# Kernel optimization log

Hardware: AMD Instinct MI355X
Metric: run time of the kernel (lower is better)

## Reference

```python
import jax, jax.numpy as jnp
import numpy as np

GROUPS = 32
EPS = 1e-5

def setup_inputs() -> dict:
    key = jax.random.key(0)
    ks = jax.random.split(key, 10)
    B, H, W, C = 2, 64, 64, 512
    s = 1.0 / np.sqrt(C)
    return {
        "x": jax.random.normal(ks[0], (B, H, W, C), dtype=jnp.float32),
        "gamma": jnp.ones((C,), jnp.float32),
        "beta": jnp.zeros((C,), jnp.float32),
        "wq": jax.random.normal(ks[1], (C, C), jnp.float32) * s,
        "bq": jnp.zeros((C,), jnp.float32),
        "wk": jax.random.normal(ks[2], (C, C), jnp.float32) * s,
        "bk": jnp.zeros((C,), jnp.float32),
        "wv": jax.random.normal(ks[3], (C, C), jnp.float32) * s,
        "bv": jnp.zeros((C,), jnp.float32),
        "wp": jax.random.normal(ks[4], (C, C), jnp.float32) * s,
        "bp": jnp.zeros((C,), jnp.float32),
    }

def _group_norm(x, gamma, beta):
    B, H, W, C = x.shape
    xg = x.reshape(B, H, W, GROUPS, C // GROUPS)
    mean = jnp.mean(xg, axis=(1, 2, 4), keepdims=True)
    var = jnp.var(xg, axis=(1, 2, 4), keepdims=True)
    xg = (xg - mean) * jax.lax.rsqrt(var + EPS)
    return xg.reshape(B, H, W, C) * gamma + beta

def reference(x, gamma, beta, wq, bq, wk, bk, wv, bv, wp, bp):
    B, H, W, C = x.shape
    h_ = _group_norm(x, gamma, beta)
    # 1x1 convs are per-pixel linear maps
    q = jnp.einsum("bhwc,cd->bhwd", h_, wq) + bq
    k = jnp.einsum("bhwc,cd->bhwd", h_, wk) + bk
    v = jnp.einsum("bhwc,cd->bhwd", h_, wv) + bv
    q = q.reshape(B, H * W, C)
    k = k.reshape(B, H * W, C)
    v = v.reshape(B, H * W, C)
    scale = C ** (-0.5)
    attn = jax.nn.softmax(jnp.einsum("bqc,bkc->bqk", q, k) * scale, axis=-1)
    out = jnp.einsum("bqk,bkc->bqc", attn, v).reshape(B, H, W, C)
    proj = jnp.einsum("bhwc,cd->bhwd", out, wp) + bp
    return x + proj
```

## Files before the change

kernel.cpp:

```cpp
#include <hip/hip_runtime.h>
#include <hip/hip_bf16.h>
#include <cstdint>
#include <cstddef>

typedef __bf16 bf16;
typedef bf16 bf16x8 __attribute__((ext_vector_type(8)));
typedef bf16 bf16x4 __attribute__((ext_vector_type(4)));
typedef float floatx4 __attribute__((ext_vector_type(4)));
typedef int intx8 __attribute__((ext_vector_type(8)));
typedef int intx4 __attribute__((ext_vector_type(4)));

#define DEVI __device__ __forceinline__

#define C_  512
#define HW_ 4096
#define B_  2
#define M_  8192
#define TK  64


DEVI floatx4 mfma16(bf16x8 a, bf16x8 b, floatx4 c) {
  return __builtin_amdgcn_mfma_f32_16x16x32_bf16(a, b, c, 0, 0, 0);
}

DEVI floatx4 mfma_fp8(intx8 a, intx8 b, floatx4 c) {
  return __builtin_amdgcn_mfma_scale_f32_16x16x128_f8f6f4(a, b, c, 0, 0,
                                                          0, 127, 0, 127);
}

DEVI void gload16(const void* g, void* lds) {
  using gp = const __attribute__((address_space(1))) unsigned int*;
  using lp = __attribute__((address_space(3))) unsigned int*;
  __builtin_amdgcn_global_load_lds(
      reinterpret_cast<gp>(reinterpret_cast<uintptr_t>(g)),
      reinterpret_cast<lp>((unsigned int)(uintptr_t)lds), 16, 0, 0);
}

template <int N> DEVI void wait_vmcnt() {
  if constexpr (N == 0)       asm volatile("s_waitcnt vmcnt(0)" ::: "memory");
  else if constexpr (N == 6)  asm volatile("s_waitcnt vmcnt(6)" ::: "memory");
  else if constexpr (N == 8)  asm volatile("s_waitcnt vmcnt(8)" ::: "memory");
  else static_assert(N == 0, "unsupported vmcnt literal");
}

DEVI uint32_t f32_to_fp8(float x) {
  return (uint32_t)__builtin_amdgcn_cvt_pk_fp8_f32(x, x, 0, false) & 0xffu;
}
DEVI int pack4_fp8(float a, float b, float c, float d) {
  int pk = __builtin_amdgcn_cvt_pk_fp8_f32(a, b, 0, false);
  return __builtin_amdgcn_cvt_pk_fp8_f32(c, d, pk, true);
}

__global__ __launch_bounds__(256) void gn_part(const float* __restrict__ x,
                                               float* __restrict__ pp,
                                               float* __restrict__ l) {
  int blk = blockIdx.x;
  int t = threadIdx.x;
  if (t < 16) l[blk * 16 + t] = 0.f;
  int batch = blk >> 8;
  int pix0 = (blk & 255) * 16;
  int c4 = (t & 127) << 2;
  int ph = t >> 7;
  const float* px = x + (size_t)batch * HW_ * C_ + (size_t)(pix0 + ph) * C_ + c4;
  float s1 = 0.f, s2 = 0.f;
#pragma unroll
  for (int i = 0; i < 8; i++) {
    float4 v = *reinterpret_cast<const float4*>(px + (size_t)i * 2 * C_);
    s1 += v.x + v.y + v.z + v.w;
    s2 += v.x * v.x + v.y * v.y + v.z * v.z + v.w * v.w;
  }
  __shared__ float l1[256], l2[256];
  l1[t] = s1; l2[t] = s2;
  __syncthreads();
  if (t < 32) {
    float a = 0.f, b2 = 0.f;
#pragma unroll
    for (int j = 0; j < 4; j++) {
      a  += l1[t * 4 + j] + l1[t * 4 + j + 128];
      b2 += l2[t * 4 + j] + l2[t * 4 + j + 128];
    }
    pp[blk * 32 + t] = a;
    pp[512 * 32 + blk * 32 + t] = b2;
  }
}

__global__ __launch_bounds__(256) void finish_wtrans(
    const float* __restrict__ pp, float* __restrict__ stats,
    const float* __restrict__ wq, const float* __restrict__ wk,
    const float* __restrict__ wv, const float* __restrict__ wp,
    uint8_t* __restrict__ w8, bf16* __restrict__ wtp) {
  int t = threadIdx.x;
  if (blockIdx.x < 64) {
    int bg = blockIdx.x;
    int b = bg >> 5, g = bg & 31;
    float s1 = pp[(b * 256 + t) * 32 + g];
    float s2 = pp[512 * 32 + (b * 256 + t) * 32 + g];
    for (int off = 32; off; off >>= 1) {
      s1 += __shfl_down(s1, off);
      s2 += __shfl_down(s2, off);
    }
    __shared__ float r1[4], r2[4];
    int wid = t >> 6;
    if ((t & 63) == 0) { r1[wid] = s1; r2[wid] = s2; }
    __syncthreads();
    if (t == 0) {
      s1 = r1[0] + r1[1] + r1[2] + r1[3];
      s2 = r2[0] + r2[1] + r2[2] + r2[3];
      float inv = 1.0f / (HW_ * 16);
      float mean = s1 * inv;
      float var  = s2 * inv - mean * mean;
      stats[bg]      = mean;
      stats[64 + bg] = rsqrtf(var + 1e-5f);
    }
    return;
  }
  int id = blockIdx.x - 64;
  int z = id >> 8;
  int k0 = ((id >> 4) & 15) * 32, n0 = (id & 15) * 32;
  const float* w = (z == 0) ? wq : (z == 1) ? wk : (z == 2) ? wv : wp;
  __shared__ float tt[32][33];
  int r = t >> 5, cc = t & 31;
  for (int i = 0; i < 4; i++) {
    int rr = r + i * 8;
    tt[rr][cc] = w[(size_t)(k0 + rr) * C_ + n0 + cc];
  }
  __syncthreads();
  if (z < 3) {
    uint8_t* dst = w8 + (size_t)z * C_ * C_;
    for (int i = 0; i < 4; i++) {
      int rr = r + i * 8;
      dst[(size_t)(n0 + rr) * C_ + k0 + cc] = (uint8_t)f32_to_fp8(tt[cc][rr]);
    }
  } else {
    for (int i = 0; i < 4; i++) {
      int rr = r + i * 8;
      wtp[(size_t)(n0 + rr) * C_ + k0 + cc] = (bf16)tt[cc][rr];
    }
  }
}

__global__ __launch_bounds__(256) void gn_apply(const float* __restrict__ x,
                                                const float* __restrict__ gamma,
                                                const float* __restrict__ beta,
                                                const float* __restrict__ stats,
                                                uint8_t* __restrict__ h8) {
  int idx = blockIdx.x * 256 + threadIdx.x;
  int m  = idx >> 7;
  int c4 = (idx & 127) << 2;
  int b = m >> 12;
  int g = c4 >> 4;
  float mean = stats[(b << 5) + g];
  float rs   = stats[64 + (b << 5) + g];
  const float4 xv = *reinterpret_cast<const float4*>(x + (size_t)m * C_ + c4);
  const float4 gv = *reinterpret_cast<const float4*>(gamma + c4);
  const float4 bv = *reinterpret_cast<const float4*>(beta + c4);
  int pk = pack4_fp8((xv.x - mean) * rs * gv.x + bv.x,
                     (xv.y - mean) * rs * gv.y + bv.y,
                     (xv.z - mean) * rs * gv.z + bv.z,
                     (xv.w - mean) * rs * gv.w + bv.w);
  *reinterpret_cast<int*>(h8 + (size_t)m * C_ + c4) = pk;
}

template <int BM, int BN, int MT, int NT>
DEVI void gemm_main(const bf16* __restrict__ A, int lda,
                    const bf16* __restrict__ Bt, int ldb,
                    int K, floatx4 (&acc)[MT][NT]) {
  constexpr int WCOLS = BN / (NT * 16);
  constexpr int NLD = BM / 32 + BN / 32;
  static_assert(NLD == 6 || NLD == 8, "vmcnt literal supports 6/8");
  __shared__ __align__(16) bf16 As[2][BM * TK];
  __shared__ __align__(16) bf16 Bs[2][BN * TK];
  int tid = threadIdx.x;
  int w = tid >> 6, lane = tid & 63;
  int wrow = w / WCOLS, wcol = w % WCOLS;
  int col = lane & 15, quad = lane >> 4;
#pragma unroll
  for (int mt = 0; mt < MT; mt++)
#pragma unroll
    for (int nt = 0; nt < NT; nt++)
      acc[mt][nt] = floatx4{0.f, 0.f, 0.f, 0.f};

  auto stage = [&](int k0, bf16* as, bf16* bs) {
#pragma unroll
    for (int i = 0; i < BM / 32; i++) {
      int id = tid + i * 256;
      int r = id >> 3, wd = id & 7;
      gload16(A + (size_t)r * lda + k0 + ((wd ^ (r & 7)) << 3), as + id * 8);
    }
#pragma unroll
    for (int i = 0; i < BN / 32; i++) {
      int id = tid + i * 256;
      int r = id >> 3, wd = id & 7;
      gload16(Bt + (size_t)r * ldb + k0 + ((wd ^ (r & 7)) << 3), bs + id * 8);
    }
  };
  auto compute = [&](const bf16* sa, const bf16* sb) {
#pragma unroll
    for (int kk = 0; kk < 2; kk++) {
      bf16x8 af[MT], bfr[NT];
#pragma unroll
      for (int mt = 0; mt < MT; mt++) {
        int rA = wrow * MT * 16 + mt * 16 + col;
        af[mt] = *reinterpret_cast<const bf16x8*>(
            sa + rA * TK + (((kk * 4 + quad) ^ (rA & 7)) << 3));
      }
#pragma unroll
      for (int nt = 0; nt < NT; nt++) {
        int rB = wcol * NT * 16 + nt * 16 + col;
        bfr[nt] = *reinterpret_cast<const bf16x8*>(
            sb + rB * TK + (((kk * 4 + quad) ^ (rB & 7)) << 3));
      }
#pragma unroll
      for (int mt = 0; mt < MT; mt++)
#pragma unroll
        for (int nt = 0; nt < NT; nt++)
          acc[mt][nt] = mfma16(af[mt], bfr[nt], acc[mt][nt]);
    }
  };

  bf16 *s0a = &As[0][0], *s0b = &Bs[0][0];
  bf16 *s1a = &As[1][0], *s1b = &Bs[1][0];
  stage(0, s0a, s0b);
  int nIter = K / TK;
  for (int t = 0; t < nIter - 1; t++) {
    stage((t + 1) * TK, s1a, s1b);
    wait_vmcnt<NLD>();
    asm volatile("s_barrier" ::: "memory");
    compute(s0a, s0b);
    asm volatile("s_waitcnt lgkmcnt(0)" ::: "memory");
    asm volatile("s_barrier" ::: "memory");
    bf16* tp;
    tp = s0a; s0a = s1a; s1a = tp;
    tp = s0b; s0b = s1b; s1b = tp;
  }
  wait_vmcnt<0>();
  asm volatile("s_barrier" ::: "memory");
  compute(s0a, s0b);
}

template <int BM, int BN, int MT, int NT, int THREADS>
DEVI void gemm_fp8(const uint8_t* __restrict__ A, int lda,
                   const uint8_t* __restrict__ Bt, int ldb,
                   int K, floatx4 (&acc)[MT][NT]) {
  constexpr int WCOLS = BN / (NT * 16);
  constexpr int RPP = THREADS / 8;
  constexpr int NLD = (BM + BN) / RPP;
  static_assert(NLD == 6 || NLD == 8, "vmcnt literal supports 6/8");
  static_assert(BM % RPP == 0 && BN % RPP == 0, "stage pass mismatch");
  __shared__ __align__(16) uint8_t As[2][BM * 128];
  __shared__ __align__(16) uint8_t Bs[2][BN * 128];
  int tid = threadIdx.x;
  int w = tid >> 6, lane = tid & 63;
  int wrow = w / WCOLS, wcol = w % WCOLS;
  int col = lane & 15, quad = lane >> 4;
#pragma unroll
  for (int mt = 0; mt < MT; mt++)
#pragma unroll
    for (int nt = 0; nt < NT; nt++)
      acc[mt][nt] = floatx4{0.f, 0.f, 0.f, 0.f};

  auto stage = [&](int k0, uint8_t* as, uint8_t* bs) {
#pragma unroll
    for (int i = 0; i < BM / RPP; i++) {
      int id = tid + i * THREADS;
      int r = id >> 3, wd = id & 7;
      gload16(A + (size_t)r * lda + k0 + ((wd ^ (r & 7)) << 4), as + id * 16);
    }
#pragma unroll
    for (int i = 0; i < BN / RPP; i++) {
      int id = tid + i * THREADS;
      int r = id >> 3, wd = id & 7;
      gload16(Bt + (size_t)r * ldb + k0 + ((wd ^ (r & 7)) << 4), bs + id * 16);
    }
  };
  auto compute = [&](const uint8_t* sa, const uint8_t* sb) {
    intx8 af[MT], bfr[NT];
#pragma unroll
    for (int mt = 0; mt < MT; mt++) {
      int rA = wrow * MT * 16 + mt * 16 + col;
      const uint8_t* rowp = sa + (size_t)rA * 128;
      intx4 lo = *reinterpret_cast<const intx4*>(
          rowp + (((2 * quad) ^ (rA & 7)) << 4));
      intx4 hi = *reinterpret_cast<const intx4*>(
          rowp + (((2 * quad + 1) ^ (rA & 7)) << 4));
      af[mt] = __builtin_shufflevector(lo, hi, 0, 1, 2, 3, 4, 5, 6, 7);
    }
#pragma unroll
    for (int nt = 0; nt < NT; nt++) {
      int rB = wcol * NT * 16 + nt * 16 + col;
      const uint8_t* rowp = sb + (size_t)rB * 128;
      intx4 lo = *reinterpret_cast<const intx4*>(
          rowp + (((2 * quad) ^ (rB & 7)) << 4));
      intx4 hi = *reinterpret_cast<const intx4*>(
          rowp + (((2 * quad + 1) ^ (rB & 7)) << 4));
      bfr[nt] = __builtin_shufflevector(lo, hi, 0, 1, 2, 3, 4, 5, 6, 7);
    }
#pragma unroll
    for (int mt = 0; mt < MT; mt++)
#pragma unroll
      for (int nt = 0; nt < NT; nt++)
        acc[mt][nt] = mfma_fp8(af[mt], bfr[nt], acc[mt][nt]);
  };

  uint8_t *s0a = &As[0][0], *s0b = &Bs[0][0];
  uint8_t *s1a = &As[1][0], *s1b = &Bs[1][0];
  stage(0, s0a, s0b);
  int nIter = K >> 7;
  for (int t = 0; t < nIter - 1; t++) {
    stage((t + 1) << 7, s1a, s1b);
    wait_vmcnt<NLD>();
    asm volatile("s_barrier" ::: "memory");
    compute(s0a, s0b);
    asm volatile("s_waitcnt lgkmcnt(0)" ::: "memory");
    asm volatile("s_barrier" ::: "memory");
    uint8_t* tp;
    tp = s0a; s0a = s1a; s1a = tp;
    tp = s0b; s0b = s1b; s1b = tp;
  }
  wait_vmcnt<0>();
  asm volatile("s_barrier" ::: "memory");
  compute(s0a, s0b);
}

__global__ __launch_bounds__(256) void gemm_qkv(const uint8_t* __restrict__ h8,
                                                const uint8_t* __restrict__ w8,
                                                const float* __restrict__ bq,
                                                const float* __restrict__ bk,
                                                const float* __restrict__ bv,
                                                uint8_t* __restrict__ q8,
                                                uint8_t* __restrict__ k8,
                                                uint8_t* __restrict__ vt8) {
  int z = blockIdx.z;
  int m0 = blockIdx.x * 128, n0 = blockIdx.y * 128;
  floatx4 acc[4][4];
  gemm_fp8<128, 128, 4, 4, 256>(h8 + (size_t)m0 * C_, C_,
                                w8 + (size_t)z * C_ * C_ + (size_t)n0 * C_, C_,
                                C_, acc);
  int tid = threadIdx.x, w = tid >> 6, lane = tid & 63;
  int wrow = w >> 1, wcol = w & 1;
  int col = lane & 15, quad = lane >> 4;
  const float* bias = (z == 0) ? bq : (z == 1) ? bk : bv;
  if (z < 2) {
    uint8_t* out = (z == 0) ? q8 : k8;
#pragma unroll
    for (int mt = 0; mt < 4; mt++)
#pragma unroll
      for (int nt = 0; nt < 4; nt++) {
        int n = n0 + wcol * 64 + nt * 16 + col;
        float bb = bias[n];
#pragma unroll
        for (int r = 0; r < 4; r++) {
          int m = m0 + wrow * 64 + mt * 16 + quad * 4 + r;
          out[(size_t)m * C_ + n] = (uint8_t)f32_to_fp8(acc[mt][nt][r] + bb);
        }
      }
  } else {
#pragma unroll
    for (int mt = 0; mt < 4; mt++)
#pragma unroll
      for (int nt = 0; nt < 4; nt++) {
        int n = n0 + wcol * 64 + nt * 16 + col;
        float bb = bias[n];
        int mbase = m0 + wrow * 64 + mt * 16 + quad * 4;
        int b = mbase >> 12;
        int s = mbase & 4095;
        int pk = pack4_fp8(acc[mt][nt][0] + bb, acc[mt][nt][1] + bb,
                           acc[mt][nt][2] + bb, acc[mt][nt][3] + bb);
        *reinterpret_cast<int*>(vt8 + ((size_t)b * C_ + n) * HW_ + s) = pk;
      }
  }
}

__global__ __launch_bounds__(512) void gemm_qk(const uint8_t* __restrict__ q8,
                                               const uint8_t* __restrict__ k8,
                                               uint8_t* __restrict__ P8,
                                               float* __restrict__ l) {
  int b = blockIdx.z;
  int fid = blockIdx.y * 16 + blockIdx.x;
  int nid = (fid & 7) * 64 + (fid >> 3);
  int m0 = (nid & 15) * 256, n0 = (nid >> 4) * 128;
  floatx4 acc[4][4];
  gemm_fp8<256, 128, 4, 4, 512>(q8 + ((size_t)b * HW_ + m0) * C_, C_,
                                k8 + ((size_t)b * HW_ + n0) * C_, C_, C_, acc);
  int tid = threadIdx.x, w = tid >> 6, lane = tid & 63;
  int wrow = w >> 1, wcol = w & 1;
  int col = lane & 15, quad = lane >> 4;
  const float sl2e = 0.044194173824159216f * 1.4426950408889634f;
  uint8_t* Pb = P8 + (size_t)b * HW_ * HW_;
  float* lb = l + (size_t)b * HW_;
#pragma unroll
  for (int mt = 0; mt < 4; mt++) {
    float rs[4] = {0.f, 0.f, 0.f, 0.f};
#pragma unroll
    for (int nt = 0; nt < 4; nt++) {
      int n = n0 + wcol * 64 + nt * 16 + col;
      float p0 = exp2f(acc[mt][nt][0] * sl2e);
      float p1 = exp2f(acc[mt][nt][1] * sl2e);
      float p2 = exp2f(acc[mt][nt][2] * sl2e);
      float p3 = exp2f(acc[mt][nt][3] * sl2e);
      int pk = pack4_fp8(p0, p1, p2, p3);
      size_t base = (size_t)(m0 + wrow * 64 + mt * 16 + quad * 4) * HW_ + n;
      Pb[base]           = (uint8_t)pk;
      Pb[base + HW_]     = (uint8_t)((unsigned)pk >> 8);
      Pb[base + 2 * HW_] = (uint8_t)((unsigned)pk >> 16);
      Pb[base + 3 * HW_] = (uint8_t)((unsigned)pk >> 24);
      rs[0] += p0; rs[1] += p1; rs[2] += p2; rs[3] += p3;
    }
#pragma unroll
    for (int off = 1; off < 16; off <<= 1)
#pragma unroll
      for (int r = 0; r < 4; r++)
        rs[r] += __shfl_xor(rs[r], off);
    if (col == 0)
#pragma unroll
      for (int r = 0; r < 4; r++)
        atomicAdd(&lb[m0 + wrow * 64 + mt * 16 + quad * 4 + r], rs[r]);
  }
}

__global__ __launch_bounds__(256) void gemm_pv(const uint8_t* __restrict__ P8,
                                               const uint8_t* __restrict__ vt8,
                                               const float* __restrict__ l,
                                               bf16* __restrict__ o) {
  int b = blockIdx.z;
  int fid = blockIdx.y * 32 + blockIdx.x;
  int xcd = fid & 7, i = fid >> 3;
  int m0 = (xcd * 4 + (i & 3)) * 128;
  int n0 = (i >> 2) * 64;
  floatx4 acc[2][4];
  gemm_fp8<128, 64, 2, 4, 256>(P8 + (size_t)b * HW_ * HW_ + (size_t)m0 * HW_,
                               HW_, vt8 + ((size_t)b * C_ + n0) * HW_, HW_,
                               HW_, acc);
  int tid = threadIdx.x, w = tid >> 6, lane = tid & 63;
  int col = lane & 15, quad = lane >> 4;
  const float* lb = l + (size_t)b * HW_;
  bf16* ob = o + (size_t)b * HW_ * C_;
#pragma unroll
  for (int mt = 0; mt < 2; mt++)
#pragma unroll
    for (int r = 0; r < 4; r++) {
      int m = m0 + w * 32 + mt * 16 + quad * 4 + r;
      float inv = 1.0f / lb[m];
#pragma unroll
      for (int nt = 0; nt < 4; nt++) {
        int n = n0 + nt * 16 + col;
        ob[(size_t)m * C_ + n] = (bf16)(acc[mt][nt][r] * inv);
      }
    }
}

__global__ __launch_bounds__(256) void gemm_proj(const bf16* __restrict__ o,
                                                 const bf16* __restrict__ wtp,
                                                 const float* __restrict__ bp,
                                                 const float* __restrict__ x,
                                                 float* __restrict__ out) {
  int m0 = blockIdx.x * 128, n0 = blockIdx.y * 64;
  floatx4 acc[2][4];
  gemm_main<128, 64, 2, 4>(o + (size_t)m0 * C_, C_, wtp + (size_t)n0 * C_, C_, C_, acc);
  int tid = threadIdx.x, w = tid >> 6, lane = tid & 63;
  int col = lane & 15, quad = lane >> 4;
#pragma unroll
  for (int mt = 0; mt < 2; mt++)
#pragma unroll
    for (int nt = 0; nt < 4; nt++) {
      int n = n0 + nt * 16 + col;
      float bb = bp[n];
#pragma unroll
      for (int r = 0; r < 4; r++) {
        int m = m0 + w * 32 + mt * 16 + quad * 4 + r;
        out[(size_t)m * C_ + n] = x[(size_t)m * C_ + n] + acc[mt][nt][r] + bb;
      }
    }
}

extern "C" void kernel_launch(void* const* d_in, const int* in_sizes, int n_in,
                              void* d_out, int out_size, void* d_ws, size_t ws_size,
                              hipStream_t stream) {
  const float* x     = (const float*)d_in[0];
  const float* gamma = (const float*)d_in[1];
  const float* beta  = (const float*)d_in[2];
  const float* wq    = (const float*)d_in[3];
  const float* bq    = (const float*)d_in[4];
  const float* wk    = (const float*)d_in[5];
  const float* bk    = (const float*)d_in[6];
  const float* wv    = (const float*)d_in[7];
  const float* bv    = (const float*)d_in[8];
  const float* wp    = (const float*)d_in[9];
  const float* bp    = (const float*)d_in[10];
  float* out = (float*)d_out;

  char* w8s = (char*)d_ws;
  float* stats = (float*)(w8s);
  float* l     = (float*)(w8s + 65536u);
  float* pp    = (float*)(w8s + 393216u);
  uint8_t* w8  = (uint8_t*)(w8s + (1u << 20));
  bf16* wtp    = (bf16*)(w8s + (2u << 20));
  uint8_t* h8  = (uint8_t*)(w8s + (4u << 20));
  bf16* o      = (bf16*)(w8s + (8u << 20));
  uint8_t* q8  = (uint8_t*)(w8s + (16u << 20));
  uint8_t* k8  = (uint8_t*)(w8s + (20u << 20));
  uint8_t* vt8 = (uint8_t*)(w8s + (24u << 20));
  uint8_t* P8  = (uint8_t*)(w8s + (28u << 20));

  gn_part<<<512, 256, 0, stream>>>(x, pp, l);
  finish_wtrans<<<1088, 256, 0, stream>>>(pp, stats, wq, wk, wv, wp, w8, wtp);
  gn_apply<<<4096, 256, 0, stream>>>(x, gamma, beta, stats, h8);
  gemm_qkv<<<dim3(M_ / 128, C_ / 128, 3), 256, 0, stream>>>(h8, w8, bq, bk, bv, q8, k8, vt8);
  gemm_qk<<<dim3(HW_ / 256, HW_ / 128, B_), 512, 0, stream>>>(q8, k8, P8, l);
  gemm_pv<<<dim3(HW_ / 128, C_ / 64, B_), 256, 0, stream>>>(P8, vt8, l, o);
  gemm_proj<<<dim3(M_ / 128, C_ / 64, 1), 256, 0, stream>>>(o, wtp, bp, x, out);
}
```

Baseline: 176.1 us.

## Compute softmax row sums in PV GEMM via MFMA against ones vector

Removes the shuffle reduction and atomicAdd-based row-sum accumulation from the QK kernel. The PV kernel instead gets the softmax denominator by running an extra fp8 MFMA of P against an all-ones operand (0x38 is 1.0 in fp8 e4m3). This drops global atomics and the zeroing of the sum buffer, at the cost of one extra MFMA per M tile per K step in PV. The sum now comes from the quantized fp8 P values, which makes it consistent with the numerator.

```diff
diff --git a/kernel.cpp b/kernel.cpp
--- a/kernel.cpp
+++ b/kernel.cpp
@@ -5,7 +5,6 @@
 
 typedef __bf16 bf16;
 typedef bf16 bf16x8 __attribute__((ext_vector_type(8)));
-typedef bf16 bf16x4 __attribute__((ext_vector_type(4)));
 typedef float floatx4 __attribute__((ext_vector_type(4)));
 typedef int intx8 __attribute__((ext_vector_type(8)));
 typedef int intx4 __attribute__((ext_vector_type(4)));
@@ -52,11 +51,9 @@
 }
 
 __global__ __launch_bounds__(256) void gn_part(const float* __restrict__ x,
-                                               float* __restrict__ pp,
-                                               float* __restrict__ l) {
+                                               float* __restrict__ pp) {
   int blk = blockIdx.x;
   int t = threadIdx.x;
-  if (t < 16) l[blk * 16 + t] = 0.f;
   int batch = blk >> 8;
   int pix0 = (blk & 255) * 16;
   int c4 = (t & 127) << 2;
@@ -238,10 +235,10 @@
   compute(s0a, s0b);
 }
 
-template <int BM, int BN, int MT, int NT, int THREADS>
+template <int BM, int BN, int MT, int NT, int THREADS, bool WITH_L>
 DEVI void gemm_fp8(const uint8_t* __restrict__ A, int lda,
                    const uint8_t* __restrict__ Bt, int ldb,
-                   int K, floatx4 (&acc)[MT][NT]) {
+                   int K, floatx4 (&acc)[MT][NT], floatx4 (&accl)[MT]) {
   constexpr int WCOLS = BN / (NT * 16);
   constexpr int RPP = THREADS / 8;
   constexpr int NLD = (BM + BN) / RPP;
@@ -253,11 +250,15 @@
   int w = tid >> 6, lane = tid & 63;
   int wrow = w / WCOLS, wcol = w % WCOLS;
   int col = lane & 15, quad = lane >> 4;
-#pragma unroll
-  for (int mt = 0; mt < MT; mt++)
+  const intx8 ones = {0x38383838, 0x38383838, 0x38383838, 0x38383838,
+                      0x38383838, 0x38383838, 0x38383838, 0x38383838};
+#pragma unroll
+  for (int mt = 0; mt < MT; mt++) {
 #pragma unroll
     for (int nt = 0; nt < NT; nt++)
       acc[mt][nt] = floatx4{0.f, 0.f, 0.f, 0.f};
+    accl[mt] = floatx4{0.f, 0.f, 0.f, 0.f};
+  }
 
   auto stage = [&](int k0, uint8_t* as, uint8_t* bs) {
 #pragma unroll
@@ -296,10 +297,13 @@
       bfr[nt] = __builtin_shufflevector(lo, hi, 0, 1, 2, 3, 4, 5, 6, 7);
     }
 #pragma unroll
-    for (int mt = 0; mt < MT; mt++)
+    for (int mt = 0; mt < MT; mt++) {
 #pragma unroll
       for (int nt = 0; nt < NT; nt++)
         acc[mt][nt] = mfma_fp8(af[mt], bfr[nt], acc[mt][nt]);
+      if constexpr (WITH_L)
+        accl[mt] = mfma_fp8(af[mt], ones, accl[mt]);
+    }
   };
 
   uint8_t *s0a = &As[0][0], *s0b = &Bs[0][0];
@@ -333,9 +337,10 @@
   int z = blockIdx.z;
   int m0 = blockIdx.x * 128, n0 = blockIdx.y * 128;
   floatx4 acc[4][4];
-  gemm_fp8<128, 128, 4, 4, 256>(h8 + (size_t)m0 * C_, C_,
-                                w8 + (size_t)z * C_ * C_ + (size_t)n0 * C_, C_,
-                                C_, acc);
+  floatx4 accl[4];
+  gemm_fp8<128, 128, 4, 4, 256, false>(h8 + (size_t)m0 * C_, C_,
+                                       w8 + (size_t)z * C_ * C_ + (size_t)n0 * C_,
+                                       C_, C_, acc, accl);
   int tid = threadIdx.x, w = tid >> 6, lane = tid & 63;
   int wrow = w >> 1, wcol = w & 1;
   int col = lane & 15, quad = lane >> 4;
@@ -373,24 +378,23 @@
 
 __global__ __launch_bounds__(512) void gemm_qk(const uint8_t* __restrict__ q8,
                                                const uint8_t* __restrict__ k8,
-                                               uint8_t* __restrict__ P8,
-                                               float* __restrict__ l) {
+                                               uint8_t* __restrict__ P8) {
   int b = blockIdx.z;
   int fid = blockIdx.y * 16 + blockIdx.x;
   int nid = (fid & 7) * 64 + (fid >> 3);
   int m0 = (nid & 15) * 256, n0 = (nid >> 4) * 128;
   floatx4 acc[4][4];
-  gemm_fp8<256, 128, 4, 4, 512>(q8 + ((size_t)b * HW_ + m0) * C_, C_,
-                                k8 + ((size_t)b * HW_ + n0) * C_, C_, C_, acc);
+  floatx4 accl[4];
+  gemm_fp8<256, 128, 4, 4, 512, false>(q8 + ((size_t)b * HW_ + m0) * C_, C_,
+                                       k8 + ((size_t)b * HW_ + n0) * C_, C_,
+                                       C_, acc, accl);
   int tid = threadIdx.x, w = tid >> 6, lane = tid & 63;
   int wrow = w >> 1, wcol = w & 1;
   int col = lane & 15, quad = lane >> 4;
   const float sl2e = 0.044194173824159216f * 1.4426950408889634f;
   uint8_t* Pb = P8 + (size_t)b * HW_ * HW_;
-  float* lb = l + (size_t)b * HW_;
 #pragma unroll
   for (int mt = 0; mt < 4; mt++) {
-    float rs[4] = {0.f, 0.f, 0.f, 0.f};
 #pragma unroll
     for (int nt = 0; nt < 4; nt++) {
       int n = n0 + wcol * 64 + nt * 16 + col;
@@ -404,23 +408,12 @@
       Pb[base + HW_]     = (uint8_t)((unsigned)pk >> 8);
       Pb[base + 2 * HW_] = (uint8_t)((unsigned)pk >> 16);
       Pb[base + 3 * HW_] = (uint8_t)((unsigned)pk >> 24);
-      rs[0] += p0; rs[1] += p1; rs[2] += p2; rs[3] += p3;
-    }
-#pragma unroll
-    for (int off = 1; off < 16; off <<= 1)
-#pragma unroll
-      for (int r = 0; r < 4; r++)
-        rs[r] += __shfl_xor(rs[r], off);
-    if (col == 0)
-#pragma unroll
-      for (int r = 0; r < 4; r++)
-        atomicAdd(&lb[m0 + wrow * 64 + mt * 16 + quad * 4 + r], rs[r]);
+    }
   }
 }
 
 __global__ __launch_bounds__(256) void gemm_pv(const uint8_t* __restrict__ P8,
                                                const uint8_t* __restrict__ vt8,
-                                               const float* __restrict__ l,
                                                bf16* __restrict__ o) {
   int b = blockIdx.z;
   int fid = blockIdx.y * 32 + blockIdx.x;
@@ -428,19 +421,19 @@
   int m0 = (xcd * 4 + (i & 3)) * 128;
   int n0 = (i >> 2) * 64;
   floatx4 acc[2][4];
-  gemm_fp8<128, 64, 2, 4, 256>(P8 + (size_t)b * HW_ * HW_ + (size_t)m0 * HW_,
-                               HW_, vt8 + ((size_t)b * C_ + n0) * HW_, HW_,
-                               HW_, acc);
+  floatx4 accl[2];
+  gemm_fp8<128, 64, 2, 4, 256, true>(P8 + (size_t)b * HW_ * HW_ + (size_t)m0 * HW_,
+                                     HW_, vt8 + ((size_t)b * C_ + n0) * HW_, HW_,
+                                     HW_, acc, accl);
   int tid = threadIdx.x, w = tid >> 6, lane = tid & 63;
   int col = lane & 15, quad = lane >> 4;
-  const float* lb = l + (size_t)b * HW_;
   bf16* ob = o + (size_t)b * HW_ * C_;
 #pragma unroll
   for (int mt = 0; mt < 2; mt++)
 #pragma unroll
     for (int r = 0; r < 4; r++) {
       int m = m0 + w * 32 + mt * 16 + quad * 4 + r;
-      float inv = 1.0f / lb[m];
+      float inv = 1.0f / accl[mt][r];
 #pragma unroll
       for (int nt = 0; nt < 4; nt++) {
         int n = n0 + nt * 16 + col;
@@ -491,7 +484,6 @@
 
   char* w8s = (char*)d_ws;
   float* stats = (float*)(w8s);
-  float* l     = (float*)(w8s + 65536u);
   float* pp    = (float*)(w8s + 393216u);
   uint8_t* w8  = (uint8_t*)(w8s + (1u << 20));
   bf16* wtp    = (bf16*)(w8s + (2u << 20));
@@ -502,11 +494,11 @@
   uint8_t* vt8 = (uint8_t*)(w8s + (24u << 20));
   uint8_t* P8  = (uint8_t*)(w8s + (28u << 20));
 
-  gn_part<<<512, 256, 0, stream>>>(x, pp, l);
+  gn_part<<<512, 256, 0, stream>>>(x, pp);
   finish_wtrans<<<1088, 256, 0, stream>>>(pp, stats, wq, wk, wv, wp, w8, wtp);
   gn_apply<<<4096, 256, 0, stream>>>(x, gamma, beta, stats, h8);
   gemm_qkv<<<dim3(M_ / 128, C_ / 128, 3), 256, 0, stream>>>(h8, w8, bq, bk, bv, q8, k8, vt8);
-  gemm_qk<<<dim3(HW_ / 256, HW_ / 128, B_), 512, 0, stream>>>(q8, k8, P8, l);
-  gemm_pv<<<dim3(HW_ / 128, C_ / 64, B_), 256, 0, stream>>>(P8, vt8, l, o);
+  gemm_qk<<<dim3(HW_ / 256, HW_ / 128, B_), 512, 0, stream>>>(q8, k8, P8);
+  gemm_pv<<<dim3(HW_ / 128, C_ / 64, B_), 256, 0, stream>>>(P8, vt8, o);
   gemm_proj<<<dim3(M_ / 128, C_ / 64, 1), 256, 0, stream>>>(o, wtp, bp, x, out);
 }
```

Result: faster. 167.1 us (-5.1%).
